# Kernel tuning notes

Measured on AMD Instinct MI355X. Metric: run time of the kernel, lower is better.

## Reference

```python
import jax, jax.numpy as jnp
import numpy as np
import math

BINS = 32  # quantization_bins


def setup_inputs() -> dict:
    key = jax.random.key(0)
    k1, k2 = jax.random.split(key)
    coords = jax.random.normal(k1, (4, 1024, 2), dtype=jnp.float32)
    # TruncatedNormal(stddev=0.02) init for the learnable table; plain normal*0.02 is fine for a numeric reference
    rpe_table = jax.random.normal(k2, (2 * BINS, 16), dtype=jnp.float32) * 0.02
    return {"coords": coords, "rpe_table": rpe_table}


def reference(coords, rpe_table):
    bins = BINS
    half = bins // 2
    eta = coords[..., 0]  # [B,T]
    phi = coords[..., 1]  # [B,T]
    rel_eta = eta[:, :, None] - eta[:, None, :]  # [B,T,T]
    rel_phi = phi[:, :, None] - phi[:, None, :]  # [B,T,T]
    pi = jnp.asarray(math.pi, dtype=phi.dtype)
    # wrap phi difference to (-pi, pi]; jnp.mod matches tf.math.floormod for floats
    rel_phi = jnp.mod(rel_phi + pi, 2 * pi) - pi
    eta_range = jnp.maximum(jnp.max(jnp.abs(rel_eta)), jnp.asarray(1e-06, eta.dtype))
    phi_range = pi
    # tf.cast float->int32 truncates toward zero, same as astype(int32)
    eta_bins = (rel_eta / eta_range * half).astype(jnp.int32)
    phi_bins = (rel_phi / phi_range * half).astype(jnp.int32)
    eta_bins = jnp.clip(eta_bins, -half, half - 1)
    phi_bins = jnp.clip(phi_bins, -half, half - 1)
    eta_idx = eta_bins + half               # [B,T,T] in [0, bins)
    phi_idx = phi_bins + half + bins        # [B,T,T] in [bins, 2*bins)
    eta_bias = rpe_table[eta_idx]           # [B,T,T,H]
    phi_bias = rpe_table[phi_idx]           # [B,T,T,H]
    bias = eta_bias + phi_bias
    return jnp.transpose(bias, (0, 3, 1, 2))  # [B,H,T,T]
```

## Files before the change

### kernel.cpp

```cpp
#include <hip/hip_runtime.h>
#include <math.h>

#define BB 4
#define TT 1024
#define HH 16
#define NROWS 64
#define RPAD 20
#define ROWS_PER_BLOCK 8

#define PI_F    3.14159265358979323846f
#define TWOPI_F 6.28318530717958647692f

typedef float f4 __attribute__((ext_vector_type(4)));

__global__ __launch_bounds__(256) void QuantizedRPE_fused_kernel(
        const float* __restrict__ coords,
        const float* __restrict__ table,
        float* __restrict__ out) {
    __shared__ float tl[NROWS][RPAD];
    __shared__ float sre[BB];
    int tid = threadIdx.x;
    int lane = tid & 63;
    int w = tid >> 6;

    {
        f4 t4 = ((const f4*)table)[tid];
        int row = tid >> 2, col = (tid & 3) * 4;
        *(f4*)&tl[row][col] = t4;
    }

    {
        const f4* cp4 = (const f4*)coords;
        float mx = -1e30f, mn = 1e30f;
        #pragma unroll
        for (int it = 0; it < TT / 128; ++it) {
            f4 v = cp4[(size_t)w * (TT / 2) + lane + it * 64];
            mx = fmaxf(mx, fmaxf(v.x, v.z));
            mn = fminf(mn, fminf(v.x, v.z));
        }
        #pragma unroll
        for (int m = 32; m; m >>= 1) {
            mx = fmaxf(mx, __shfl_xor(mx, m));
            mn = fminf(mn, __shfl_xor(mn, m));
        }
        if (lane == 0) sre[w] = mx - mn;
    }
    __syncthreads();
    float range = fmaxf(fmaxf(fmaxf(sre[0], sre[1]), fmaxf(sre[2], sre[3])), 1e-6f);

    int b  = blockIdx.x >> 7;
    int i0 = (blockIdx.x & 127) * ROWS_PER_BLOCK;

    int j0 = tid * 4;
    const f4* cp = (const f4*)(coords + (size_t)(b * TT + j0) * 2);
    f4 c01 = cp[0];
    f4 c23 = cp[1];
    float ej[4] = {c01.x, c01.z, c23.x, c23.z};
    float pj[4] = {c01.y, c01.w, c23.y, c23.w};

    #pragma unroll
    for (int r = 0; r < ROWS_PER_BLOCK; ++r) {
        int i = i0 + r;
        float ei  = coords[(size_t)(b * TT + i) * 2 + 0];
        float pii = coords[(size_t)(b * TT + i) * 2 + 1];

        float s[4][16];
        #pragma unroll
        for (int jj = 0; jj < 4; ++jj) {
            float re = ei - ej[jj];
            int be = (int)(re / range * 16.0f);
            be = min(max(be, -16), 15);
            int eidx = be + 16;
            float ww = (pii - pj[jj]) + PI_F;
            float m = fmodf(ww, TWOPI_F);
            if (m < 0.0f) m += TWOPI_F;
            float rp = m - PI_F;
            int bp = (int)(rp / PI_F * 16.0f);
            bp = min(max(bp, -16), 15);
            int pidx = bp + 48;

            const f4* er = (const f4*)&tl[eidx][0];
            const f4* pr = (const f4*)&tl[pidx][0];
            #pragma unroll
            for (int q = 0; q < 4; ++q) {
                f4 a = er[q];
                f4 c = pr[q];
                s[jj][q * 4 + 0] = a.x + c.x;
                s[jj][q * 4 + 1] = a.y + c.y;
                s[jj][q * 4 + 2] = a.z + c.z;
                s[jj][q * 4 + 3] = a.w + c.w;
            }
        }

        float* op = out + ((size_t)(b * HH) * TT + i) * TT + j0;
        #pragma unroll
        for (int h = 0; h < HH; ++h) {
            f4 v = {s[0][h], s[1][h], s[2][h], s[3][h]};
            *(f4*)(op + (size_t)h * TT * TT) = v;
        }
    }
}

extern "C" void kernel_launch(void* const* d_in, const int* in_sizes, int n_in,
                              void* d_out, int out_size, void* d_ws, size_t ws_size,
                              hipStream_t stream) {
    const float* coords = (const float*)d_in[0];
    const float* table  = (const float*)d_in[1];
    float* out = (float*)d_out;
    (void)d_ws; (void)ws_size;

    QuantizedRPE_fused_kernel<<<BB * TT / ROWS_PER_BLOCK, 256, 0, stream>>>(coords, table, out);
}
```

Baseline: 46.34 us.

## Split heads across waves and widen per-lane column coverage

After: 99.27 us. +114.2%, slower.

```diff
diff --git a/kernel.cpp b/kernel.cpp
--- a/kernel.cpp
+++ b/kernel.cpp
@@ -51,12 +51,17 @@
     int b  = blockIdx.x >> 7;
     int i0 = (blockIdx.x & 127) * ROWS_PER_BLOCK;
 
-    int j0 = tid * 4;
-    const f4* cp = (const f4*)(coords + (size_t)(b * TT + j0) * 2);
-    f4 c01 = cp[0];
-    f4 c23 = cp[1];
-    float ej[4] = {c01.x, c01.z, c23.x, c23.z};
-    float pj[4] = {c01.y, c01.w, c23.y, c23.w};
+    float ej[16], pj[16];
+    #pragma unroll
+    for (int c = 0; c < 4; ++c) {
+        const f4* cp = (const f4*)(coords + (size_t)(b * TT + c * 256 + lane * 4) * 2);
+        f4 c01 = cp[0];
+        f4 c23 = cp[1];
+        ej[c * 4 + 0] = c01.x; pj[c * 4 + 0] = c01.y;
+        ej[c * 4 + 1] = c01.z; pj[c * 4 + 1] = c01.w;
+        ej[c * 4 + 2] = c23.x; pj[c * 4 + 2] = c23.y;
+        ej[c * 4 + 3] = c23.z; pj[c * 4 + 3] = c23.w;
+    }
 
     #pragma unroll
     for (int r = 0; r < ROWS_PER_BLOCK; ++r) {
@@ -64,9 +69,9 @@
         float ei  = coords[(size_t)(b * TT + i) * 2 + 0];
         float pii = coords[(size_t)(b * TT + i) * 2 + 1];
 
-        float s[4][16];
+        float v[16][4];
         #pragma unroll
-        for (int jj = 0; jj < 4; ++jj) {
+        for (int jj = 0; jj < 16; ++jj) {
             float re = ei - ej[jj];
             int be = (int)(re / range * 16.0f);
             be = min(max(be, -16), 15);
@@ -79,24 +84,24 @@
             bp = min(max(bp, -16), 15);
             int pidx = bp + 48;
 
-            const f4* er = (const f4*)&tl[eidx][0];
-            const f4* pr = (const f4*)&tl[pidx][0];
-            #pragma unroll
-            for (int q = 0; q < 4; ++q) {
-                f4 a = er[q];
-                f4 c = pr[q];
-                s[jj][q * 4 + 0] = a.x + c.x;
-                s[jj][q * 4 + 1] = a.y + c.y;
-                s[jj][q * 4 + 2] = a.z + c.z;
-                s[jj][q * 4 + 3] = a.w + c.w;
-            }
+            f4 a = *(const f4*)&tl[eidx][4 * w];
+            f4 p = *(const f4*)&tl[pidx][4 * w];
+            v[jj][0] = a.x + p.x;
+            v[jj][1] = a.y + p.y;
+            v[jj][2] = a.z + p.z;
+            v[jj][3] = a.w + p.w;
         }
 
-        float* op = out + ((size_t)(b * HH) * TT + i) * TT + j0;
+        float* rowp = out + ((size_t)(b * HH + 4 * w) * TT + i) * TT + lane * 4;
         #pragma unroll
-        for (int h = 0; h < HH; ++h) {
-            f4 v = {s[0][h], s[1][h], s[2][h], s[3][h]};
-            *(f4*)(op + (size_t)h * TT * TT) = v;
+        for (int q = 0; q < 4; ++q) {
+            float* hp = rowp + (size_t)q * TT * TT;
+            #pragma unroll
+            for (int c = 0; c < 4; ++c) {
+                f4 sv = { v[c * 4 + 0][q], v[c * 4 + 1][q],
+                          v[c * 4 + 2][q], v[c * 4 + 3][q] };
+                *(f4*)(hp + c * 256) = sv;
+            }
         }
     }
 }
```
